# Kernel optimization log

Hardware: AMD Instinct MI355X
Metric: run time of the kernel (lower is better)

## Reference

```python
import jax, jax.numpy as jnp
import numpy as np

EMBED_DIM = 1024
N_HEADS = 16
DK = EMBED_DIM // N_HEADS


def setup_inputs() -> dict:
    key = jax.random.key(0)
    ks = jax.random.split(key, 9)
    s = 1.0 / np.sqrt(EMBED_DIM)
    d = EMBED_DIM
    return {
        "x": jax.random.normal(ks[0], (2, 2048, d), dtype=jnp.float32),
        "Wq": jax.random.uniform(ks[1], (d, d), jnp.float32, -s, s),
        "bq": jax.random.uniform(ks[2], (d,), jnp.float32, -s, s),
        "Wk": jax.random.uniform(ks[3], (d, d), jnp.float32, -s, s),
        "bk": jax.random.uniform(ks[4], (d,), jnp.float32, -s, s),
        "Wv": jax.random.uniform(ks[5], (d, d), jnp.float32, -s, s),
        "bv": jax.random.uniform(ks[6], (d,), jnp.float32, -s, s),
        "Wo": jax.random.uniform(ks[7], (d, d), jnp.float32, -s, s),
        "bo": jax.random.uniform(ks[8], (d,), jnp.float32, -s, s),
    }


def reference(x, Wq, bq, Wk, bk, Wv, bv, Wo, bo):
    B, S, D = x.shape
    H, dk = N_HEADS, DK
    # QKV projections
    q = (x @ Wq + bq).reshape(B, S, H, dk).transpose(0, 2, 1, 3)  # [B,H,S,dk]
    k = (x @ Wk + bk).reshape(B, S, H, dk).transpose(0, 2, 1, 3)
    v = (x @ Wv + bv).reshape(B, S, H, dk).transpose(0, 2, 1, 3)
    # scaled dot-product attention with full score matrix (faithful to source)
    scores = jnp.einsum("bhqd,bhkd->bhqk", q, k) / jnp.sqrt(jnp.float32(dk))
    attn = jax.nn.softmax(scores, axis=-1)
    out = jnp.einsum("bhqk,bhkd->bhqd", attn, v)  # [B,H,S,dk]
    out = out.transpose(0, 2, 1, 3).reshape(B, S, D)
    return out @ Wo + bo
```

## Files before the change

kernel.cpp:

```cpp
#include <hip/hip_runtime.h>

typedef unsigned short u16;
typedef unsigned int u32;
typedef __attribute__((ext_vector_type(8))) short short8;
typedef __attribute__((ext_vector_type(4))) float float4v;
typedef __attribute__((ext_vector_type(4))) unsigned int uint4v;

struct alignas(8) U16x4 { u16 x, y, z, w; };

__device__ __forceinline__ u16 f2b(float f) {
    union { float f; unsigned int u; } v; v.f = f;
    unsigned int r = (v.u >> 16) & 1u;
    v.u += 0x7fffu + r;
    return (u16)(v.u >> 16);
}

__device__ __forceinline__ float b2f(u16 u) {
    union { unsigned int u; float f; } v; v.u = ((u32)u) << 16; return v.f;
}

__device__ __forceinline__ void gld16(const u16* g, u16* l) {
    __builtin_amdgcn_global_load_lds(
        (const __attribute__((address_space(1))) void*)g,
        (__attribute__((address_space(3))) void*)l, 16, 0, 0);
}

__device__ __forceinline__ short8 frag8(const u16* base, int row, int cg) {
    return *(const short8*)(base + row * 64 + ((cg ^ (row & 7)) << 3));
}

__global__ __launch_bounds__(256) void prep_kernel(
    const float* __restrict__ x, const float* __restrict__ W0,
    const float* __restrict__ W1, const float* __restrict__ W2,
    const float* __restrict__ W3, u16* __restrict__ xb,
    u16* __restrict__ T0, u16* __restrict__ T1,
    u16* __restrict__ T2, u16* __restrict__ T3) {
    __shared__ float tile[32][33];
    int id = blockIdx.x;
    if (id < 4096) {
        size_t i = ((size_t)id * 256 + threadIdx.x) * 4;
        float4 v = *(const float4*)(x + i);
        U16x4 o;
        o.x = f2b(v.x); o.y = f2b(v.y); o.z = f2b(v.z); o.w = f2b(v.w);
        *(U16x4*)(xb + i) = o;
        return;
    }
    int r = id - 4096;
    int z = r >> 10, tl = r & 1023;
    const float* W = (z == 0) ? W0 : (z == 1) ? W1 : (z == 2) ? W2 : W3;
    u16* T = (z == 0) ? T0 : (z == 1) ? T1 : (z == 2) ? T2 : T3;
    int t = threadIdx.x;
    int tx = t & 31, ty = t >> 5;
    int bn = (tl & 31) * 32, bk = (tl >> 5) * 32;
#pragma unroll
    for (int p = 0; p < 4; ++p) {
        int k = ty + p * 8;
        tile[k][tx] = W[(size_t)(bk + k) * 1024 + bn + tx];
    }
    __syncthreads();
#pragma unroll
    for (int p = 0; p < 4; ++p) {
        int n = ty + p * 8;
        T[(size_t)(bn + n) * 1024 + bk + tx] = f2b(tile[tx][n]);
    }
}

__global__ __launch_bounds__(512, 2) void qkv_kernel(
    const u16* __restrict__ X,
    const u16* __restrict__ WqT, const u16* __restrict__ WkT, const u16* __restrict__ WvT,
    const float* __restrict__ bq, const float* __restrict__ bk, const float* __restrict__ bv,
    u16* __restrict__ Qo, u16* __restrict__ Ko, u16* __restrict__ VTo) {
    __shared__ __align__(16) u16 As[128 * 64];
    __shared__ __align__(16) u16 Bs[3][128 * 64];
    int id = blockIdx.x;
    int m = (id & 7) | (((id >> 3) & 3) << 3);
    int n = id >> 5;
    int t = threadIdx.x;
    int m0 = m * 128, n0 = n * 128;
    int lane = t & 63, wid = t >> 6;
    int wr = wid >> 2, wc = wid & 3;
    int l16 = lane & 15, quad = lane >> 4;
    int rl = lane >> 3, cs = lane & 7;

    int tileid = wid >> 1, half = wid & 1;
    const u16* gsrc = (tileid == 0) ? X : (tileid == 1) ? WqT
                     : (tileid == 2) ? WkT : WvT;
    int gbase = (tileid == 0) ? m0 : n0;
    u16* ldst = (tileid == 0) ? As : &Bs[tileid - 1][0];

    float4v acc[3][4][2];
    float4v zero4 = {0.f, 0.f, 0.f, 0.f};
#pragma unroll
    for (int z = 0; z < 3; ++z)
#pragma unroll
        for (int i = 0; i < 4; ++i)
#pragma unroll
            for (int j = 0; j < 2; ++j) acc[z][i][j] = zero4;

    for (int k0 = 0; k0 < 1024; k0 += 64) {
        __syncthreads();
#pragma unroll
        for (int p = 0; p < 8; ++p) {
            int q = half * 8 + p;
            int row = q * 8 + rl;
            int c = cs ^ (row & 7);
            gld16(gsrc + (size_t)(gbase + row) * 1024 + k0 + c * 8, ldst + q * 512);
        }
        __syncthreads();
#pragma unroll
        for (int ks = 0; ks < 64; ks += 32) {
            int cg = (ks >> 3) + quad;
            short8 af[4];
#pragma unroll
            for (int i = 0; i < 4; ++i)
                af[i] = frag8(As, wr * 64 + i * 16 + l16, cg);
#pragma unroll
            for (int z = 0; z < 3; ++z) {
                short8 bf[2];
#pragma unroll
                for (int j = 0; j < 2; ++j)
                    bf[j] = frag8(&Bs[z][0], wc * 32 + j * 16 + l16, cg);
#pragma unroll
                for (int i = 0; i < 4; ++i)
#pragma unroll
                    for (int j = 0; j < 2; ++j)
                        acc[z][i][j] = __builtin_amdgcn_mfma_f32_16x16x32_bf16(
                            af[i], bf[j], acc[z][i][j], 0, 0, 0);
            }
        }
    }

    const float QSCALE = 0.18033688011112042f;
#pragma unroll
    for (int j = 0; j < 2; ++j) {
        int n1 = n0 + wc * 32 + j * 16 + l16;
        float bql = bq[n1], bkl = bk[n1], bvl = bv[n1];
#pragma unroll
        for (int i = 0; i < 4; ++i) {
            int mbase = m0 + wr * 64 + i * 16 + quad * 4;
#pragma unroll
            for (int r = 0; r < 4; ++r) {
                Qo[(size_t)(mbase + r) * 1024 + n1] =
                    f2b((acc[0][i][j][r] + bql) * QSCALE);
                Ko[(size_t)(mbase + r) * 1024 + n1] =
                    f2b(acc[1][i][j][r] + bkl);
            }
            int bidx = mbase >> 11, s = mbase & 2047;
            size_t base =
                ((size_t)((bidx * 16 + (n1 >> 6)) * 64 + (n1 & 63))) * 2048 + s;
            U16x4 pk;
            pk.x = f2b(acc[2][i][j][0] + bvl);
            pk.y = f2b(acc[2][i][j][1] + bvl);
            pk.z = f2b(acc[2][i][j][2] + bvl);
            pk.w = f2b(acc[2][i][j][3] + bvl);
            *(U16x4*)(VTo + base) = pk;
        }
    }
}

__global__ __launch_bounds__(256) void oproj_kernel(const u16* __restrict__ X,
                                                    const u16* __restrict__ WoT,
                                                    const float* __restrict__ bias,
                                                    float* __restrict__ out) {
    __shared__ __align__(16) u16 As[64 * 64];
    __shared__ __align__(16) u16 Bs[128 * 64];
    int id = blockIdx.x;
    int m = (id & 7) | (((id >> 3) & 7) << 3);
    int n = id >> 6;
    int t = threadIdx.x;
    int m0 = m * 64, n0 = n * 128;
    int lane = t & 63, wid = t >> 6;
    int l16 = lane & 15, quad = lane >> 4;
    int rl = lane >> 3, cs = lane & 7;

    float4v acc[4][2];
    float4v zero4 = {0.f, 0.f, 0.f, 0.f};
#pragma unroll
    for (int i = 0; i < 4; ++i)
#pragma unroll
        for (int j = 0; j < 2; ++j) acc[i][j] = zero4;

    for (int k0 = 0; k0 < 1024; k0 += 64) {
        __syncthreads();
#pragma unroll
        for (int p = 0; p < 2; ++p) {
            int blk = wid * 2 + p;
            int row = blk * 8 + rl;
            int c = cs ^ (row & 7);
            gld16(X + (size_t)(m0 + row) * 1024 + k0 + c * 8, As + blk * 512);
        }
#pragma unroll
        for (int p = 0; p < 4; ++p) {
            int blk = wid * 4 + p;
            int row = blk * 8 + rl;
            int c = cs ^ (row & 7);
            gld16(WoT + (size_t)(n0 + row) * 1024 + k0 + c * 8, Bs + blk * 512);
        }
        __syncthreads();
#pragma unroll
        for (int ks = 0; ks < 64; ks += 32) {
            int cg = (ks >> 3) + quad;
            short8 af[4], bf[2];
#pragma unroll
            for (int i = 0; i < 4; ++i) af[i] = frag8(As, i * 16 + l16, cg);
#pragma unroll
            for (int j = 0; j < 2; ++j) bf[j] = frag8(Bs, wid * 32 + j * 16 + l16, cg);
#pragma unroll
            for (int i = 0; i < 4; ++i)
#pragma unroll
                for (int j = 0; j < 2; ++j)
                    acc[i][j] = __builtin_amdgcn_mfma_f32_16x16x32_bf16(
                        af[i], bf[j], acc[i][j], 0, 0, 0);
        }
    }

#pragma unroll
    for (int j = 0; j < 2; ++j) {
        int n1 = n0 + wid * 32 + j * 16 + l16;
        float bvl = bias[n1];
#pragma unroll
        for (int i = 0; i < 4; ++i) {
            int mbase = m0 + i * 16 + quad * 4;
#pragma unroll
            for (int r = 0; r < 4; ++r)
                out[(size_t)(mbase + r) * 1024 + n1] = acc[i][j][r] + bvl;
        }
    }
}

__global__ __launch_bounds__(256, 4) void flash_kernel(const u16* __restrict__ Q,
                                                       const u16* __restrict__ Kn,
                                                       const u16* __restrict__ VT,
                                                       u16* __restrict__ Opart,
                                                       float* __restrict__ lpart) {
    __shared__ __align__(16) u16 Ks[2][64 * 64];
    __shared__ __align__(16) u16 Vs[2][64 * 64];

    int id = blockIdx.x;
    int bh = (id & 7) | (((id >> 3) & 3) << 3);
    int rest = id >> 5;
    int qb = rest & 15, kvz = rest >> 4;
    int b = bh >> 4, h = bh & 15;
    int t = threadIdx.x;
    int wid = t >> 6, lane = t & 63;
    int l16 = lane & 15, quad = lane >> 4;
    int rl = lane >> 3, cs = lane & 7;
    int q0 = qb * 128 + wid * 32;
    size_t kbase = (size_t)(b * 2048) * 1024 + h * 64;
    size_t vbase = (size_t)(bh * 64) * 2048;
    int kv0 = kvz * 1024;

    short8 qf[2][2];
#pragma unroll
    for (int j = 0; j < 2; ++j)
#pragma unroll
        for (int kk = 0; kk < 2; ++kk)
            qf[j][kk] = *(const short8*)(
                Q + ((size_t)(b * 2048 + q0 + j * 16 + l16)) * 1024 + h * 64 +
                kk * 32 + quad * 8);

    float4v oacc[2][4];
    float lreg[2];
    float4v zero4 = {0.f, 0.f, 0.f, 0.f};
#pragma unroll
    for (int ip = 0; ip < 2; ++ip) {
        lreg[ip] = 0.f;
#pragma unroll
        for (int jd = 0; jd < 4; ++jd) oacc[ip][jd] = zero4;
    }

#define STAGE_KV(buf, kv)                                                     \
    {                                                                         \
        _Pragma("unroll") for (int p2 = 0; p2 < 2; ++p2) {                    \
            int p = wid * 2 + p2;                                             \
            int row = p * 8 + rl;                                             \
            int c = cs ^ (row & 7);                                           \
            int key = (((row >> 4) & 1) << 5) | (((row >> 2) & 3) << 3) |     \
                      (((row >> 5) & 1) << 2) | (row & 3);                    \
            gld16(Kn + kbase + (size_t)((kv) + key) * 1024 + c * 8,           \
                  &Ks[buf][p * 512]);                                         \
            gld16(VT + vbase + (size_t)row * 2048 + (kv) + c * 8,             \
                  &Vs[buf][p * 512]);                                         \
        }                                                                     \
    }

    STAGE_KV(0, kv0);

    for (int kvi = 0; kvi < 16; ++kvi) {
        int buf = kvi & 1;
        __syncthreads();
        if (kvi + 1 < 16) STAGE_KV(buf ^ 1, kv0 + (kvi + 1) * 64);

        u32 pw[2][4][2];
#pragma unroll
        for (int i = 0; i < 4; ++i) {
            float4v s0 = zero4, s1 = zero4;
            __builtin_amdgcn_s_setprio(1);
#pragma unroll
            for (int kk = 0; kk < 2; ++kk) {
                short8 kf = frag8(&Ks[buf][0], i * 16 + l16, kk * 4 + quad);
                s0 = __builtin_amdgcn_mfma_f32_16x16x32_bf16(kf, qf[0][kk], s0, 0, 0, 0);
                s1 = __builtin_amdgcn_mfma_f32_16x16x32_bf16(kf, qf[1][kk], s1, 0, 0, 0);
            }
            __builtin_amdgcn_s_setprio(0);
#pragma unroll
            for (int j = 0; j < 2; ++j) {
                float4v s = (j == 0) ? s0 : s1;
                float e0f = __builtin_amdgcn_exp2f(s[0]);
                float e1f = __builtin_amdgcn_exp2f(s[1]);
                float e2f = __builtin_amdgcn_exp2f(s[2]);
                float e3f = __builtin_amdgcn_exp2f(s[3]);
                lreg[j] += (e0f + e1f) + (e2f + e3f);
                u32 e0 = __float_as_uint(e0f) + 0x8000u;
                u32 e1 = __float_as_uint(e1f) + 0x8000u;
                u32 e2 = __float_as_uint(e2f) + 0x8000u;
                u32 e3 = __float_as_uint(e3f) + 0x8000u;
                pw[j][i][0] = __builtin_amdgcn_perm(e1, e0, 0x07060302u);
                pw[j][i][1] = __builtin_amdgcn_perm(e3, e2, 0x07060302u);
            }
        }

        __builtin_amdgcn_s_setprio(1);
#pragma unroll
        for (int kk = 0; kk < 2; ++kk) {
            int cg = kk * 4 + quad;
            short8 vf[4];
#pragma unroll
            for (int jd = 0; jd < 4; ++jd)
                vf[jd] = frag8(&Vs[buf][0], jd * 16 + l16, cg);
#pragma unroll
            for (int j = 0; j < 2; ++j) {
                union { uint4v u; short8 s; } pu;
                pu.u = (uint4v){pw[j][kk][0], pw[j][kk][1],
                                pw[j][2 + kk][0], pw[j][2 + kk][1]};
#pragma unroll
                for (int jd = 0; jd < 4; ++jd)
                    oacc[j][jd] = __builtin_amdgcn_mfma_f32_16x16x32_bf16(
                        pu.s, vf[jd], oacc[j][jd], 0, 0, 0);
            }
        }
        __builtin_amdgcn_s_setprio(0);
    }
#undef STAGE_KV

#pragma unroll
    for (int j = 0; j < 2; ++j) {
        lreg[j] += __shfl_xor(lreg[j], 16);
        lreg[j] += __shfl_xor(lreg[j], 32);
    }

    size_t obase = (size_t)kvz * 4194304;
#pragma unroll
    for (int ip = 0; ip < 2; ++ip)
#pragma unroll
        for (int r = 0; r < 4; ++r) {
            int q = q0 + ip * 16 + quad * 4 + r;
#pragma unroll
            for (int jd = 0; jd < 4; ++jd)
                Opart[obase + ((size_t)(b * 2048 + q)) * 1024 + h * 64 +
                      jd * 16 + l16] = f2b(oacc[ip][jd][r]);
        }
    if (quad == 0) {
#pragma unroll
        for (int j = 0; j < 2; ++j) {
            int q = q0 + j * 16 + l16;
            lpart[kvz * 65536 + (b * 2048 + q) * 16 + h] = lreg[j];
        }
    }
}

__global__ __launch_bounds__(256) void combine_kernel(const u16* __restrict__ Op,
                                                      const float* __restrict__ lp,
                                                      u16* __restrict__ out) {
    int idx = blockIdx.x * 256 + threadIdx.x;
    size_t i = (size_t)idx * 4;
    int qg = idx >> 8;
    int d = (idx & 255) * 4;
    int h = d >> 6;
    float l0 = lp[qg * 16 + h], l1 = lp[65536 + qg * 16 + h];
    float inv = 1.0f / (l0 + l1);
    U16x4 o0 = *(const U16x4*)(Op + i);
    U16x4 o1 = *(const U16x4*)(Op + 4194304 + i);
    U16x4 o;
    o.x = f2b((b2f(o0.x) + b2f(o1.x)) * inv);
    o.y = f2b((b2f(o0.y) + b2f(o1.y)) * inv);
    o.z = f2b((b2f(o0.z) + b2f(o1.z)) * inv);
    o.w = f2b((b2f(o0.w) + b2f(o1.w)) * inv);
    *(U16x4*)(out + i) = o;
}

extern "C" void kernel_launch(void* const* d_in, const int* in_sizes, int n_in,
                              void* d_out, int out_size, void* d_ws, size_t ws_size,
                              hipStream_t stream) {
    const float* x  = (const float*)d_in[0];
    const float* Wq = (const float*)d_in[1];
    const float* bq = (const float*)d_in[2];
    const float* Wk = (const float*)d_in[3];
    const float* bk = (const float*)d_in[4];
    const float* Wv = (const float*)d_in[5];
    const float* bv = (const float*)d_in[6];
    const float* Wo = (const float*)d_in[7];
    const float* bo = (const float*)d_in[8];
    float* out = (float*)d_out;

    char* ws = (char*)d_ws;
    const size_t MB = 1024 * 1024;
    u16* xb  = (u16*)(ws);
    u16* wqt = (u16*)(ws + 8 * MB);
    u16* wkt = (u16*)(ws + 10 * MB);
    u16* wvt = (u16*)(ws + 12 * MB);
    u16* wot = (u16*)(ws + 14 * MB);
    u16* qb_ = (u16*)(ws + 16 * MB);
    u16* kb_ = (u16*)(ws + 24 * MB);
    u16* vt_ = (u16*)(ws + 32 * MB);
    u16* ab_ = (u16*)(ws + 40 * MB);
    u16* op_ = (u16*)(ws + 48 * MB);
    float* lp_ = (float*)(ws + 64 * MB);

    prep_kernel<<<8192, 256, 0, stream>>>(x, Wq, Wk, Wv, Wo, xb,
                                          wqt, wkt, wvt, wot);
    qkv_kernel<<<256, 512, 0, stream>>>(xb, wqt, wkt, wvt, bq, bk, bv,
                                        qb_, kb_, vt_);
    flash_kernel<<<1024, 256, 0, stream>>>(qb_, kb_, vt_, op_, lp_);
    combine_kernel<<<4096, 256, 0, stream>>>(op_, lp_, ab_);
    oproj_kernel<<<512, 256, 0, stream>>>(ab_, wot, bo, out);
}
```

Before: 189.4 us.

## Shrink projection GEMM tiles, compute softmax denominator via MFMA, use packed bf16 convert

The QKV projection tile shrinks from 128x128 to 64x128 rows, with 8 waves each owning 16 output columns. That doubles the grid to 512 blocks and raises the launch-bounds occupancy target. The output projection tile drops to 64x64, also doubling its grid, so more blocks fill the CUs. In the flash kernel, P is packed to bf16 with the hardware v_cvt_pk_bf16_f32 instruction instead of manual add-and-permute. The softmax row sum is now an extra MFMA against a vector of ones instead of VALU adds plus cross-lane shuffles. Smaller tiles add redundant global/LDS loads per FLOP, and the extra MFMA adds matrix-core work per step.

After: 177.4 us. 1.07x faster.

```diff
diff --git a/kernel.cpp b/kernel.cpp
--- a/kernel.cpp
+++ b/kernel.cpp
@@ -17,6 +17,12 @@
 
 __device__ __forceinline__ float b2f(u16 u) {
     union { unsigned int u; float f; } v; v.u = ((u32)u) << 16; return v.f;
+}
+
+__device__ __forceinline__ u32 cvt_pk_bf16(float lo, float hi) {
+    u32 d;
+    asm("v_cvt_pk_bf16_f32 %0, %1, %2" : "=v"(d) : "v"(lo), "v"(hi));
+    return d;
 }
 
 __device__ __forceinline__ void gld16(const u16* g, u16* l) {
@@ -65,105 +71,13 @@
     }
 }
 
-__global__ __launch_bounds__(512, 2) void qkv_kernel(
+__global__ __launch_bounds__(512, 4) void qkv_kernel(
     const u16* __restrict__ X,
     const u16* __restrict__ WqT, const u16* __restrict__ WkT, const u16* __restrict__ WvT,
     const float* __restrict__ bq, const float* __restrict__ bk, const float* __restrict__ bv,
     u16* __restrict__ Qo, u16* __restrict__ Ko, u16* __restrict__ VTo) {
-    __shared__ __align__(16) u16 As[128 * 64];
+    __shared__ __align__(16) u16 As[64 * 64];
     __shared__ __align__(16) u16 Bs[3][128 * 64];
-    int id = blockIdx.x;
-    int m = (id & 7) | (((id >> 3) & 3) << 3);
-    int n = id >> 5;
-    int t = threadIdx.x;
-    int m0 = m * 128, n0 = n * 128;
-    int lane = t & 63, wid = t >> 6;
-    int wr = wid >> 2, wc = wid & 3;
-    int l16 = lane & 15, quad = lane >> 4;
-    int rl = lane >> 3, cs = lane & 7;
-
-    int tileid = wid >> 1, half = wid & 1;
-    const u16* gsrc = (tileid == 0) ? X : (tileid == 1) ? WqT
-                     : (tileid == 2) ? WkT : WvT;
-    int gbase = (tileid == 0) ? m0 : n0;
-    u16* ldst = (tileid == 0) ? As : &Bs[tileid - 1][0];
-
-    float4v acc[3][4][2];
-    float4v zero4 = {0.f, 0.f, 0.f, 0.f};
-#pragma unroll
-    for (int z = 0; z < 3; ++z)
-#pragma unroll
-        for (int i = 0; i < 4; ++i)
-#pragma unroll
-            for (int j = 0; j < 2; ++j) acc[z][i][j] = zero4;
-
-    for (int k0 = 0; k0 < 1024; k0 += 64) {
-        __syncthreads();
-#pragma unroll
-        for (int p = 0; p < 8; ++p) {
-            int q = half * 8 + p;
-            int row = q * 8 + rl;
-            int c = cs ^ (row & 7);
-            gld16(gsrc + (size_t)(gbase + row) * 1024 + k0 + c * 8, ldst + q * 512);
-        }
-        __syncthreads();
-#pragma unroll
-        for (int ks = 0; ks < 64; ks += 32) {
-            int cg = (ks >> 3) + quad;
-            short8 af[4];
-#pragma unroll
-            for (int i = 0; i < 4; ++i)
-                af[i] = frag8(As, wr * 64 + i * 16 + l16, cg);
-#pragma unroll
-            for (int z = 0; z < 3; ++z) {
-                short8 bf[2];
-#pragma unroll
-                for (int j = 0; j < 2; ++j)
-                    bf[j] = frag8(&Bs[z][0], wc * 32 + j * 16 + l16, cg);
-#pragma unroll
-                for (int i = 0; i < 4; ++i)
-#pragma unroll
-                    for (int j = 0; j < 2; ++j)
-                        acc[z][i][j] = __builtin_amdgcn_mfma_f32_16x16x32_bf16(
-                            af[i], bf[j], acc[z][i][j], 0, 0, 0);
-            }
-        }
-    }
-
-    const float QSCALE = 0.18033688011112042f;
-#pragma unroll
-    for (int j = 0; j < 2; ++j) {
-        int n1 = n0 + wc * 32 + j * 16 + l16;
-        float bql = bq[n1], bkl = bk[n1], bvl = bv[n1];
-#pragma unroll
-        for (int i = 0; i < 4; ++i) {
-            int mbase = m0 + wr * 64 + i * 16 + quad * 4;
-#pragma unroll
-            for (int r = 0; r < 4; ++r) {
-                Qo[(size_t)(mbase + r) * 1024 + n1] =
-                    f2b((acc[0][i][j][r] + bql) * QSCALE);
-                Ko[(size_t)(mbase + r) * 1024 + n1] =
-                    f2b(acc[1][i][j][r] + bkl);
-            }
-            int bidx = mbase >> 11, s = mbase & 2047;
-            size_t base =
-                ((size_t)((bidx * 16 + (n1 >> 6)) * 64 + (n1 & 63))) * 2048 + s;
-            U16x4 pk;
-            pk.x = f2b(acc[2][i][j][0] + bvl);
-            pk.y = f2b(acc[2][i][j][1] + bvl);
-            pk.z = f2b(acc[2][i][j][2] + bvl);
-            pk.w = f2b(acc[2][i][j][3] + bvl);
-            *(U16x4*)(VTo + base) = pk;
-        }
-    }
-}
-
-__global__ __launch_bounds__(256) void oproj_kernel(const u16* __restrict__ X,
-                                                    const u16* __restrict__ WoT,
-                                                    const float* __restrict__ bias,
-                                                    float* __restrict__ out) {
-    __shared__ __align__(16) u16 As[64 * 64];
-    __shared__ __align__(16) u16 Bs[128 * 64];
     int id = blockIdx.x;
     int m = (id & 7) | (((id >> 3) & 7) << 3);
     int n = id >> 6;
@@ -173,12 +87,99 @@
     int l16 = lane & 15, quad = lane >> 4;
     int rl = lane >> 3, cs = lane & 7;
 
-    float4v acc[4][2];
+    int z_st = (wid - 2) >> 1, half = wid & 1;
+    const u16* gsrcB = (z_st == 0) ? WqT : (z_st == 1) ? WkT : WvT;
+
+    float4v acc[3][4];
     float4v zero4 = {0.f, 0.f, 0.f, 0.f};
 #pragma unroll
-    for (int i = 0; i < 4; ++i)
-#pragma unroll
-        for (int j = 0; j < 2; ++j) acc[i][j] = zero4;
+    for (int z = 0; z < 3; ++z)
+#pragma unroll
+        for (int i = 0; i < 4; ++i) acc[z][i] = zero4;
+
+    for (int k0 = 0; k0 < 1024; k0 += 64) {
+        __syncthreads();
+        if (wid < 2) {
+#pragma unroll
+            for (int p = 0; p < 4; ++p) {
+                int q = wid * 4 + p;
+                int row = q * 8 + rl;
+                int c = cs ^ (row & 7);
+                gld16(X + (size_t)(m0 + row) * 1024 + k0 + c * 8, As + q * 512);
+            }
+        } else {
+#pragma unroll
+            for (int p = 0; p < 8; ++p) {
+                int q = half * 8 + p;
+                int row = q * 8 + rl;
+                int c = cs ^ (row & 7);
+                gld16(gsrcB + (size_t)(n0 + row) * 1024 + k0 + c * 8,
+                      &Bs[z_st][0] + q * 512);
+            }
+        }
+        __syncthreads();
+#pragma unroll
+        for (int ks = 0; ks < 64; ks += 32) {
+            int cg = (ks >> 3) + quad;
+            short8 af[4];
+#pragma unroll
+            for (int i = 0; i < 4; ++i)
+                af[i] = frag8(As, i * 16 + l16, cg);
+#pragma unroll
+            for (int z = 0; z < 3; ++z) {
+                short8 bf = frag8(&Bs[z][0], wid * 16 + l16, cg);
+#pragma unroll
+                for (int i = 0; i < 4; ++i)
+                    acc[z][i] = __builtin_amdgcn_mfma_f32_16x16x32_bf16(
+                        af[i], bf, acc[z][i], 0, 0, 0);
+            }
+        }
+    }
+
+    const float QSCALE = 0.18033688011112042f;
+    int n1 = n0 + wid * 16 + l16;
+    float bql = bq[n1], bkl = bk[n1], bvl = bv[n1];
+#pragma unroll
+    for (int i = 0; i < 4; ++i) {
+        int mbase = m0 + i * 16 + quad * 4;
+#pragma unroll
+        for (int r = 0; r < 4; ++r) {
+            Qo[(size_t)(mbase + r) * 1024 + n1] =
+                f2b((acc[0][i][r] + bql) * QSCALE);
+            Ko[(size_t)(mbase + r) * 1024 + n1] =
+                f2b(acc[1][i][r] + bkl);
+        }
+        int bidx = mbase >> 11, s = mbase & 2047;
+        size_t base =
+            ((size_t)((bidx * 16 + (n1 >> 6)) * 64 + (n1 & 63))) * 2048 + s;
+        U16x4 pk;
+        pk.x = f2b(acc[2][i][0] + bvl);
+        pk.y = f2b(acc[2][i][1] + bvl);
+        pk.z = f2b(acc[2][i][2] + bvl);
+        pk.w = f2b(acc[2][i][3] + bvl);
+        *(U16x4*)(VTo + base) = pk;
+    }
+}
+
+__global__ __launch_bounds__(256, 4) void oproj_kernel(const u16* __restrict__ X,
+                                                       const u16* __restrict__ WoT,
+                                                       const float* __restrict__ bias,
+                                                       float* __restrict__ out) {
+    __shared__ __align__(16) u16 As[64 * 64];
+    __shared__ __align__(16) u16 Bs[64 * 64];
+    int id = blockIdx.x;
+    int m = (id & 7) | (((id >> 3) & 7) << 3);
+    int n = id >> 6;
+    int t = threadIdx.x;
+    int m0 = m * 64, n0 = n * 64;
+    int lane = t & 63, wid = t >> 6;
+    int l16 = lane & 15, quad = lane >> 4;
+    int rl = lane >> 3, cs = lane & 7;
+
+    float4v acc[4];
+    float4v zero4 = {0.f, 0.f, 0.f, 0.f};
+#pragma unroll
+    for (int i = 0; i < 4; ++i) acc[i] = zero4;
 
     for (int k0 = 0; k0 < 1024; k0 += 64) {
         __syncthreads();
@@ -188,43 +189,31 @@
             int row = blk * 8 + rl;
             int c = cs ^ (row & 7);
             gld16(X + (size_t)(m0 + row) * 1024 + k0 + c * 8, As + blk * 512);
-        }
-#pragma unroll
-        for (int p = 0; p < 4; ++p) {
-            int blk = wid * 4 + p;
-            int row = blk * 8 + rl;
-            int c = cs ^ (row & 7);
             gld16(WoT + (size_t)(n0 + row) * 1024 + k0 + c * 8, Bs + blk * 512);
         }
         __syncthreads();
 #pragma unroll
         for (int ks = 0; ks < 64; ks += 32) {
             int cg = (ks >> 3) + quad;
-            short8 af[4], bf[2];
+            short8 af[4];
 #pragma unroll
             for (int i = 0; i < 4; ++i) af[i] = frag8(As, i * 16 + l16, cg);
-#pragma unroll
-            for (int j = 0; j < 2; ++j) bf[j] = frag8(Bs, wid * 32 + j * 16 + l16, cg);
+            short8 bf = frag8(Bs, wid * 16 + l16, cg);
 #pragma unroll
             for (int i = 0; i < 4; ++i)
-#pragma unroll
-                for (int j = 0; j < 2; ++j)
-                    acc[i][j] = __builtin_amdgcn_mfma_f32_16x16x32_bf16(
-                        af[i], bf[j], acc[i][j], 0, 0, 0);
-        }
-    }
-
-#pragma unroll
-    for (int j = 0; j < 2; ++j) {
-        int n1 = n0 + wid * 32 + j * 16 + l16;
-        float bvl = bias[n1];
-#pragma unroll
-        for (int i = 0; i < 4; ++i) {
-            int mbase = m0 + i * 16 + quad * 4;
-#pragma unroll
-            for (int r = 0; r < 4; ++r)
-                out[(size_t)(mbase + r) * 1024 + n1] = acc[i][j][r] + bvl;
-        }
+                acc[i] = __builtin_amdgcn_mfma_f32_16x16x32_bf16(
+                    af[i], bf, acc[i], 0, 0, 0);
+        }
+    }
+
+    int n1 = n0 + wid * 16 + l16;
+    float bvl = bias[n1];
+#pragma unroll
+    for (int i = 0; i < 4; ++i) {
+        int mbase = m0 + i * 16 + quad * 4;
+#pragma unroll
+        for (int r = 0; r < 4; ++r)
+            out[(size_t)(mbase + r) * 1024 + n1] = acc[i][r] + bvl;
     }
 }
 
@@ -260,11 +249,13 @@
                 kk * 32 + quad * 8);
 
     float4v oacc[2][4];
-    float lreg[2];
+    float4v den[2];
     float4v zero4 = {0.f, 0.f, 0.f, 0.f};
+    const short8 ones8 = {(short)0x3F80, (short)0x3F80, (short)0x3F80, (short)0x3F80,
+                          (short)0x3F80, (short)0x3F80, (short)0x3F80, (short)0x3F80};
 #pragma unroll
     for (int ip = 0; ip < 2; ++ip) {
-        lreg[ip] = 0.f;
+        den[ip] = zero4;
 #pragma unroll
         for (int jd = 0; jd < 4; ++jd) oacc[ip][jd] = zero4;
     }
@@ -310,13 +301,8 @@
                 float e1f = __builtin_amdgcn_exp2f(s[1]);
                 float e2f = __builtin_amdgcn_exp2f(s[2]);
                 float e3f = __builtin_amdgcn_exp2f(s[3]);
-                lreg[j] += (e0f + e1f) + (e2f + e3f);
-                u32 e0 = __float_as_uint(e0f) + 0x8000u;
-                u32 e1 = __float_as_uint(e1f) + 0x8000u;
-                u32 e2 = __float_as_uint(e2f) + 0x8000u;
-                u32 e3 = __float_as_uint(e3f) + 0x8000u;
-                pw[j][i][0] = __builtin_amdgcn_perm(e1, e0, 0x07060302u);
-                pw[j][i][1] = __builtin_amdgcn_perm(e3, e2, 0x07060302u);
+                pw[j][i][0] = cvt_pk_bf16(e0f, e1f);
+                pw[j][i][1] = cvt_pk_bf16(e2f, e3f);
             }
         }
 
@@ -337,17 +323,13 @@
                 for (int jd = 0; jd < 4; ++jd)
                     oacc[j][jd] = __builtin_amdgcn_mfma_f32_16x16x32_bf16(
                         pu.s, vf[jd], oacc[j][jd], 0, 0, 0);
+                den[j] = __builtin_amdgcn_mfma_f32_16x16x32_bf16(
+                    pu.s, ones8, den[j], 0, 0, 0);
             }
         }
         __builtin_amdgcn_s_setprio(0);
     }
 #undef STAGE_KV
-
-#pragma unroll
-    for (int j = 0; j < 2; ++j) {
-        lreg[j] += __shfl_xor(lreg[j], 16);
-        lreg[j] += __shfl_xor(lreg[j], 32);
-    }
 
     size_t obase = (size_t)kvz * 4194304;
 #pragma unroll
@@ -360,12 +342,14 @@
                 Opart[obase + ((size_t)(b * 2048 + q)) * 1024 + h * 64 +
                       jd * 16 + l16] = f2b(oacc[ip][jd][r]);
         }
-    if (quad == 0) {
-#pragma unroll
-        for (int j = 0; j < 2; ++j) {
-            int q = q0 + j * 16 + l16;
-            lpart[kvz * 65536 + (b * 2048 + q) * 16 + h] = lreg[j];
-        }
+    if (l16 == 0) {
+#pragma unroll
+        for (int j = 0; j < 2; ++j)
+#pragma unroll
+            for (int r = 0; r < 4; ++r) {
+                int q = q0 + j * 16 + quad * 4 + r;
+                lpart[kvz * 65536 + (b * 2048 + q) * 16 + h] = den[j][r];
+            }
     }
 }
 
@@ -419,9 +403,9 @@
 
     prep_kernel<<<8192, 256, 0, stream>>>(x, Wq, Wk, Wv, Wo, xb,
                                           wqt, wkt, wvt, wot);
-    qkv_kernel<<<256, 512, 0, stream>>>(xb, wqt, wkt, wvt, bq, bk, bv,
+    qkv_kernel<<<512, 512, 0, stream>>>(xb, wqt, wkt, wvt, bq, bk, bv,
                                         qb_, kb_, vt_);
     flash_kernel<<<1024, 256, 0, stream>>>(qb_, kb_, vt_, op_, lp_);
     combine_kernel<<<4096, 256, 0, stream>>>(op_, lp_, ab_);
-    oproj_kernel<<<512, 256, 0, stream>>>(ab_, wot, bo, out);
-}
+    oproj_kernel<<<1024, 256, 0, stream>>>(ab_, wot, bo, out);
+}
```
